# Performance work log

Measured on AMD Instinct MI355X. Metric: run time of the kernel, lower is better.

Reference implementation:

```python
import jax, jax.numpy as jnp
import numpy as np
from jax import lax

B, H, N, F = 32, 168, 512, 8
P_STEPS = 24


def setup_inputs() -> dict:
    key = jax.random.key(0)
    ks = jax.random.split(key, 8)
    s = 0.02
    return {
        "x": jax.random.normal(ks[0], (B, H, N, F), dtype=jnp.float32),
        "conv_w": jax.random.normal(ks[1], (N * F, N), dtype=jnp.float32) * s,
        "conv_b": jnp.zeros((N,), dtype=jnp.float32),
        "lstm_k": jax.random.normal(ks[2], (N, 4 * N), dtype=jnp.float32) * s,
        "lstm_rk": jax.random.normal(ks[3], (N, 4 * N), dtype=jnp.float32) * s,
        "lstm_b": jnp.zeros((4 * N,), dtype=jnp.float32),
        "dense_w": jax.random.normal(ks[4], (N, N), dtype=jnp.float32) * s,
        "dense_b": jnp.zeros((N,), dtype=jnp.float32),
        "P": P_STEPS,
    }


def _lstm_cell(h, c, x_t, lstm_k, lstm_rk, lstm_b):
    # Keras LSTMCell gate order: i, f, g(candidate), o
    z = x_t @ lstm_k + h @ lstm_rk + lstm_b  # [B, 4N]
    i, f, g, o = jnp.split(z, 4, axis=-1)
    i = jax.nn.sigmoid(i)
    f = jax.nn.sigmoid(f)
    g = jnp.tanh(g)
    o = jax.nn.sigmoid(o)
    c_new = f * c + i * g
    h_new = o * jnp.tanh(c_new)
    return h_new, c_new


def reference(x, conv_w, conv_b, lstm_k, lstm_rk, lstm_b, dense_w, dense_b, P):
    b, hh, n, f = x.shape
    # Conv1D kernel_size=1 == per-timestep dense projection N*F -> N
    xr = x.reshape(b, hh, n * f) @ conv_w + conv_b  # [B, H, N]

    h0 = jnp.zeros((b, n), dtype=x.dtype)
    c0 = jnp.zeros((b, n), dtype=x.dtype)

    def enc_step(carry, x_t):
        h, c = carry
        h, c = _lstm_cell(h, c, x_t, lstm_k, lstm_rk, lstm_b)
        return (h, c), None

    (h, c), _ = lax.scan(enc_step, (h0, c0), xr.transpose(1, 0, 2))

    def dec_step(carry, _):
        h, c = carry
        h2, c2 = _lstm_cell(h, c, h, lstm_k, lstm_rk, lstm_b)
        return (h2, c2), h2

    _, preds = lax.scan(dec_step, (h, c), None, length=P)  # [P, B, N]
    preds = preds.transpose(1, 0, 2)  # [B, P, N]
    return preds @ dense_w + dense_b
```

## Files before the change

### kernel.cpp

```cpp
#include <hip/hip_runtime.h>
#include <hip/hip_bf16.h>
#include <math.h>

typedef __hip_bfloat16 bf16;
typedef __attribute__((ext_vector_type(8))) short short8;
typedef __attribute__((ext_vector_type(4))) float floatx4;

#define B_  32
#define H_  168
#define N_  512
#define P_  24
#define NF_ 4096
#define G4N 2048
#define M1  (B_*H_)
#define NX  (M1*NF_)
#define TSTEPS (H_+P_)
#define NWG 64
#define HSZ (B_*N_)

__global__ __launch_bounds__(256) void cvt_f32_bf16(const float* __restrict__ in,
                                                    bf16* __restrict__ out, int n4) {
  int i = blockIdx.x * 256 + threadIdx.x;
  if (i < n4) {
    float4 v = ((const float4*)in)[i];
    bf16 o[4] = {__float2bfloat16(v.x), __float2bfloat16(v.y),
                 __float2bfloat16(v.z), __float2bfloat16(v.w)};
    *(ulong1*)(out + (size_t)i * 4) = *(ulong1*)o;
  }
}

__global__ __launch_bounds__(256) void transpose_cvt(const float* __restrict__ in,
                                                     bf16* __restrict__ out,
                                                     int R, int C) {
  __shared__ float t[32][33];
  int bx = blockIdx.x, by = blockIdx.y;
  int tx = threadIdx.x, ty = threadIdx.y;
#pragma unroll
  for (int yy = 0; yy < 32; yy += 8)
    t[ty + yy][tx] = in[(size_t)(by * 32 + ty + yy) * C + bx * 32 + tx];
  __syncthreads();
#pragma unroll
  for (int yy = 0; yy < 32; yy += 8)
    out[(size_t)(bx * 32 + ty + yy) * R + by * 32 + tx] =
        __float2bfloat16(t[tx][ty + yy]);
}

__global__ __launch_bounds__(256) void transpose_add_cvt(const float* __restrict__ in1,
                                                         const float* __restrict__ in2,
                                                         bf16* __restrict__ out,
                                                         int R, int C) {
  __shared__ float t[32][33];
  int bx = blockIdx.x, by = blockIdx.y;
  int tx = threadIdx.x, ty = threadIdx.y;
#pragma unroll
  for (int yy = 0; yy < 32; yy += 8) {
    size_t idx = (size_t)(by * 32 + ty + yy) * C + bx * 32 + tx;
    t[ty + yy][tx] = in1[idx] + in2[idx];
  }
  __syncthreads();
#pragma unroll
  for (int yy = 0; yy < 32; yy += 8)
    out[(size_t)(bx * 32 + ty + yy) * R + by * 32 + tx] =
        __float2bfloat16(t[tx][ty + yy]);
}

template <bool OUT_BF16>
__global__ __launch_bounds__(256) void gemm_bt(const bf16* __restrict__ A,
                                               const bf16* __restrict__ BT,
                                               const float* __restrict__ bias,
                                               void* __restrict__ Cout,
                                               int M, int N, int K, int permute) {
  __shared__ short As[128 * 40];
  __shared__ short Bs[128 * 40];
  int tid  = threadIdx.x;
  int wave = tid >> 6, lane = tid & 63;
  int wm = wave >> 1, wn = wave & 1;
  int quad = lane >> 4, l16 = lane & 15;
  int m0 = blockIdx.y * 128, n0 = blockIdx.x * 128;

  floatx4 acc[4][4];
#pragma unroll
  for (int i = 0; i < 4; i++)
#pragma unroll
    for (int j = 0; j < 4; j++) acc[i][j] = (floatx4){0.f, 0.f, 0.f, 0.f};

  int r0 = tid >> 2;
  int c0 = (tid & 3) * 8;

  for (int k0 = 0; k0 < K; k0 += 32) {
    short8 a0 = *(const short8*)(A  + (size_t)(m0 + r0)      * K + k0 + c0);
    short8 a1 = *(const short8*)(A  + (size_t)(m0 + r0 + 64) * K + k0 + c0);
    short8 b0 = *(const short8*)(BT + (size_t)(n0 + r0)      * K + k0 + c0);
    short8 b1 = *(const short8*)(BT + (size_t)(n0 + r0 + 64) * K + k0 + c0);
    __syncthreads();
    *(short8*)(&As[r0 * 40 + c0])        = a0;
    *(short8*)(&As[(r0 + 64) * 40 + c0]) = a1;
    *(short8*)(&Bs[r0 * 40 + c0])        = b0;
    *(short8*)(&Bs[(r0 + 64) * 40 + c0]) = b1;
    __syncthreads();
    short8 af[4], bfr[4];
#pragma unroll
    for (int i = 0; i < 4; i++)
      af[i] = *(const short8*)(&As[(wm * 64 + i * 16 + l16) * 40 + quad * 8]);
#pragma unroll
    for (int j = 0; j < 4; j++)
      bfr[j] = *(const short8*)(&Bs[(wn * 64 + j * 16 + l16) * 40 + quad * 8]);
#pragma unroll
    for (int i = 0; i < 4; i++)
#pragma unroll
      for (int j = 0; j < 4; j++)
        acc[i][j] = __builtin_amdgcn_mfma_f32_16x16x32_bf16(af[i], bfr[j],
                                                            acc[i][j], 0, 0, 0);
  }
#pragma unroll
  for (int i = 0; i < 4; i++) {
    int row = m0 + wm * 64 + i * 16 + quad * 4;
#pragma unroll
    for (int j = 0; j < 4; j++) {
      int col = n0 + wn * 64 + j * 16 + l16;
      float bv = bias ? bias[col] : 0.f;
#pragma unroll
      for (int r = 0; r < 4; r++) {
        int gr = row + r;
        int orow = permute ? (gr % H_) * B_ + gr / H_ : gr;
        float v = acc[i][j][r] + bv;
        if (OUT_BF16)
          ((bf16*)Cout)[(size_t)orow * N + col] = __float2bfloat16(v);
        else
          ((float*)Cout)[(size_t)orow * N + col] = v;
      }
    }
  }
}

__global__ __launch_bounds__(256) void lstm_persist(
    const bf16* __restrict__ rkT,
    const bf16* __restrict__ wcT,
    const float* __restrict__ bvec,
    const float* __restrict__ xk,
    bf16* __restrict__ hring,
    bf16* __restrict__ preds,
    unsigned* __restrict__ bar,
    unsigned* __restrict__ flag) {
  __shared__ short Wenc[32][520];
  __shared__ short Wdec[32][520];
  __shared__ float zs[32][33];
  __shared__ bf16  hstage[32][8];

  int tid  = threadIdx.x;
  int wave = tid >> 6, lane = tid & 63;
  int tm = wave >> 1, tn = wave & 1;
  int quad = lane >> 4, l16 = lane & 15;
  int n0 = blockIdx.x * 8;
  int lc   = tn * 16 + l16;
  int gcol = ((lc >> 3) << 9) + n0 + (lc & 7);
  int brow = tm * 16 + quad * 4;

  for (int idx = tid; idx < 32 * 64; idx += 256) {
    int r = idx >> 6, ck = (idx & 63) << 3;
    int grow = ((r >> 3) << 9) + n0 + (r & 7);
    *(short8*)&Wenc[r][ck] = *(const short8*)(rkT + (size_t)grow * 512 + ck);
    *(short8*)&Wdec[r][ck] = *(const short8*)(wcT + (size_t)grow * 512 + ck);
  }
  float bias_r = bvec[gcol];
  int b = tid >> 3, j = tid & 7;
  int nn = n0 + j;
  float c_reg = 0.f;

  float xkv[4];
  {
    const float* xp = xk + (size_t)brow * G4N + gcol;
#pragma unroll
    for (int r = 0; r < 4; ++r) xkv[r] = xp[(size_t)r * G4N];
  }
  __syncthreads();

  for (int t = 0; t < TSTEPS; ++t) {
    const bf16* h_in = hring + (size_t)t * HSZ;
    bf16*       h_out = hring + (size_t)(t + 1) * HSZ;
    const short(*Ws)[520] = (t < H_) ? Wenc : Wdec;

    floatx4 acc0 = (floatx4){0.f, 0.f, 0.f, 0.f};
    floatx4 acc1 = (floatx4){0.f, 0.f, 0.f, 0.f};
    const bf16*  ap = h_in + (size_t)(tm * 16 + l16) * 512 + quad * 8;
    const short* bp = &Ws[lc][quad * 8];
#pragma unroll
    for (int k0 = 0; k0 < 512; k0 += 64) {
      short8 av0 = *(const short8*)(ap + k0);
      short8 av1 = *(const short8*)(ap + k0 + 32);
      short8 bv0 = *(const short8*)(bp + k0);
      short8 bv1 = *(const short8*)(bp + k0 + 32);
      acc0 = __builtin_amdgcn_mfma_f32_16x16x32_bf16(av0, bv0, acc0, 0, 0, 0);
      acc1 = __builtin_amdgcn_mfma_f32_16x16x32_bf16(av1, bv1, acc1, 0, 0, 0);
    }
    floatx4 acc = acc0 + acc1;
#pragma unroll
    for (int r = 0; r < 4; ++r)
      zs[brow + r][lc] = acc[r] + bias_r + xkv[r];

    float xn[4] = {0.f, 0.f, 0.f, 0.f};
    if (t + 1 < H_) {
      const float* xp = xk + (size_t)((t + 1) * B_ + brow) * G4N + gcol;
#pragma unroll
      for (int r = 0; r < 4; ++r) xn[r] = xp[(size_t)r * G4N];
    }
    __syncthreads();

    float zi = zs[b][j], zf = zs[b][8 + j], zg = zs[b][16 + j], zo = zs[b][24 + j];
    float ig = 1.f / (1.f + __expf(-zi));
    float fg = 1.f / (1.f + __expf(-zf));
    float gg = tanhf(zg);
    float og = 1.f / (1.f + __expf(-zo));
    c_reg = fg * c_reg + ig * gg;
    float hn = og * tanhf(c_reg);
    hstage[b][j] = __float2bfloat16(hn);
    if (t >= H_)
      preds[(size_t)b * (P_ * N_) + (t - H_) * N_ + nn] = __float2bfloat16(hn);
    __syncthreads();

    if (tid < 64) {
      int bb = tid >> 1, f4 = (tid & 1) * 4;
      unsigned long long v = *(const unsigned long long*)&hstage[bb][f4];
      __hip_atomic_store((unsigned long long*)(h_out + bb * 512 + n0 + f4), v,
                         __ATOMIC_RELAXED, __HIP_MEMORY_SCOPE_AGENT);
    }
    __syncthreads();

    if (tid == 0) {
      unsigned old = __hip_atomic_fetch_add(&bar[t], 1u, __ATOMIC_RELAXED,
                                            __HIP_MEMORY_SCOPE_AGENT);
      if (old == NWG - 1) {
        __hip_atomic_store(&flag[t], 1u, __ATOMIC_RELAXED,
                           __HIP_MEMORY_SCOPE_AGENT);
      } else {
        while (!__hip_atomic_load(&flag[t], __ATOMIC_RELAXED,
                                  __HIP_MEMORY_SCOPE_AGENT))
          __builtin_amdgcn_s_sleep(1);
      }
    }
    __builtin_amdgcn_fence(__ATOMIC_ACQUIRE, "workgroup");
    __syncthreads();
#pragma unroll
    for (int r = 0; r < 4; ++r) xkv[r] = xn[r];
  }
}

extern "C" void kernel_launch(void* const* d_in, const int* in_sizes, int n_in,
                              void* d_out, int out_size, void* d_ws, size_t ws_size,
                              hipStream_t stream) {
  const float* x       = (const float*)d_in[0];
  const float* conv_w  = (const float*)d_in[1];
  const float* conv_b  = (const float*)d_in[2];
  const float* lstm_k  = (const float*)d_in[3];
  const float* lstm_rk = (const float*)d_in[4];
  const float* lstm_b  = (const float*)d_in[5];
  const float* dense_w = (const float*)d_in[6];
  const float* dense_b = (const float*)d_in[7];
  float* out = (float*)d_out;

  char* p = (char*)d_ws;
  auto carve = [&](size_t bytes) {
    char* r = p;
    p += (bytes + 255) & ~(size_t)255;
    return r;
  };
  bf16*  xb    = (bf16*)carve((size_t)NX * 2);
  bf16*  xr    = (bf16*)carve((size_t)M1 * N_ * 2);
  float* xk    = (float*)carve((size_t)M1 * G4N * 4);
  bf16*  cwT   = (bf16*)carve((size_t)N_ * NF_ * 2);
  bf16*  kT    = (bf16*)carve((size_t)G4N * N_ * 2);
  bf16*  rkT   = (bf16*)carve((size_t)G4N * N_ * 2);
  bf16*  wcT   = (bf16*)carve((size_t)G4N * N_ * 2);
  bf16*  dwT   = (bf16*)carve((size_t)N_ * N_ * 2);
  bf16*  preds = (bf16*)carve((size_t)B_ * P_ * N_ * 2);
  bf16*  hring = (bf16*)carve((size_t)(TSTEPS + 1) * HSZ * 2);
  unsigned* bar  = (unsigned*)carve((size_t)TSTEPS * 4);
  unsigned* flag = (unsigned*)carve((size_t)TSTEPS * 4);

  cvt_f32_bf16<<<(NX / 4 + 255) / 256, 256, 0, stream>>>(x, xb, NX / 4);
  dim3 tb(32, 8);
  transpose_cvt<<<dim3(N_ / 32, NF_ / 32), tb, 0, stream>>>(conv_w, cwT, NF_, N_);
  transpose_cvt<<<dim3(G4N / 32, N_ / 32), tb, 0, stream>>>(lstm_k, kT, N_, G4N);
  transpose_cvt<<<dim3(G4N / 32, N_ / 32), tb, 0, stream>>>(lstm_rk, rkT, N_, G4N);
  transpose_add_cvt<<<dim3(G4N / 32, N_ / 32), tb, 0, stream>>>(lstm_k, lstm_rk,
                                                                wcT, N_, G4N);
  transpose_cvt<<<dim3(N_ / 32, N_ / 32), tb, 0, stream>>>(dense_w, dwT, N_, N_);
  hipMemsetAsync(hring, 0, (size_t)HSZ * 2, stream);
  hipMemsetAsync(bar, 0, (size_t)TSTEPS * 4, stream);
  hipMemsetAsync(flag, 0, (size_t)TSTEPS * 4, stream);

  gemm_bt<true><<<dim3(N_ / 128, M1 / 128), 256, 0, stream>>>(xb, cwT, conv_b, xr,
                                                              M1, N_, NF_, 1);
  gemm_bt<false><<<dim3(G4N / 128, M1 / 128), 256, 0, stream>>>(xr, kT, nullptr,
                                                                xk, M1, G4N, N_, 0);

  lstm_persist<<<NWG, 256, 0, stream>>>(rkT, wcT, lstm_b, xk, hring, preds,
                                        bar, flag);

  gemm_bt<false><<<dim3(N_ / 128, (B_ * P_) / 128), 256, 0, stream>>>(
      preds, dwT, dense_b, out, B_ * P_, N_, N_, 0);
}
```

Before: 1.065 ms.

## Replace atomic-counter grid barrier with per-wave byte flags polled in parallel

Each wave now writes its h values directly with per-element atomic stores and then sets its own byte flag for the step. One wave of every workgroup polls all 256 flags as 64 packed words, one per lane. This replaces the LDS staging, two block syncs, the serialized fetch_add counter and the single release flag. The next-step xk prefetch is moved to after the flag write so its latency overlaps the barrier wait. In exchange the h writes are 2-byte scattered atomic stores instead of 8-byte ones, and correctness relies on s_waitcnt ordering the data stores before the flag store.

```diff
diff --git a/kernel.cpp b/kernel.cpp
--- a/kernel.cpp
+++ b/kernel.cpp
@@ -140,12 +140,10 @@
     const float* __restrict__ xk,
     bf16* __restrict__ hring,
     bf16* __restrict__ preds,
-    unsigned* __restrict__ bar,
-    unsigned* __restrict__ flag) {
+    unsigned char* __restrict__ flg) {
   __shared__ short Wenc[32][520];
   __shared__ short Wdec[32][520];
   __shared__ float zs[32][33];
-  __shared__ bf16  hstage[32][8];
 
   int tid  = threadIdx.x;
   int wave = tid >> 6, lane = tid & 63;
@@ -176,7 +174,7 @@
   __syncthreads();
 
   for (int t = 0; t < TSTEPS; ++t) {
-    const bf16* h_in = hring + (size_t)t * HSZ;
+    const bf16* h_in  = hring + (size_t)t * HSZ;
     bf16*       h_out = hring + (size_t)(t + 1) * HSZ;
     const short(*Ws)[520] = (t < H_) ? Wenc : Wdec;
 
@@ -197,13 +195,6 @@
 #pragma unroll
     for (int r = 0; r < 4; ++r)
       zs[brow + r][lc] = acc[r] + bias_r + xkv[r];
-
-    float xn[4] = {0.f, 0.f, 0.f, 0.f};
-    if (t + 1 < H_) {
-      const float* xp = xk + (size_t)((t + 1) * B_ + brow) * G4N + gcol;
-#pragma unroll
-      for (int r = 0; r < 4; ++r) xn[r] = xp[(size_t)r * G4N];
-    }
     __syncthreads();
 
     float zi = zs[b][j], zf = zs[b][8 + j], zg = zs[b][16 + j], zo = zs[b][24 + j];
@@ -213,30 +204,31 @@
     float og = 1.f / (1.f + __expf(-zo));
     c_reg = fg * c_reg + ig * gg;
     float hn = og * tanhf(c_reg);
-    hstage[b][j] = __float2bfloat16(hn);
+    bf16 hv = __float2bfloat16(hn);
+    unsigned short hu = *(unsigned short*)&hv;
+    __hip_atomic_store((unsigned short*)h_out + (size_t)b * 512 + nn, hu,
+                       __ATOMIC_RELAXED, __HIP_MEMORY_SCOPE_AGENT);
     if (t >= H_)
-      preds[(size_t)b * (P_ * N_) + (t - H_) * N_ + nn] = __float2bfloat16(hn);
-    __syncthreads();
-
-    if (tid < 64) {
-      int bb = tid >> 1, f4 = (tid & 1) * 4;
-      unsigned long long v = *(const unsigned long long*)&hstage[bb][f4];
-      __hip_atomic_store((unsigned long long*)(h_out + bb * 512 + n0 + f4), v,
-                         __ATOMIC_RELAXED, __HIP_MEMORY_SCOPE_AGENT);
-    }
-    __syncthreads();
-
-    if (tid == 0) {
-      unsigned old = __hip_atomic_fetch_add(&bar[t], 1u, __ATOMIC_RELAXED,
-                                            __HIP_MEMORY_SCOPE_AGENT);
-      if (old == NWG - 1) {
-        __hip_atomic_store(&flag[t], 1u, __ATOMIC_RELAXED,
-                           __HIP_MEMORY_SCOPE_AGENT);
-      } else {
-        while (!__hip_atomic_load(&flag[t], __ATOMIC_RELAXED,
-                                  __HIP_MEMORY_SCOPE_AGENT))
-          __builtin_amdgcn_s_sleep(1);
-      }
+      preds[(size_t)b * (P_ * N_) + (t - H_) * N_ + nn] = hv;
+
+    asm volatile("s_waitcnt vmcnt(0)" ::: "memory");
+    if (lane == 0)
+      __hip_atomic_store(flg + (size_t)t * 256 + blockIdx.x * 4 + wave,
+                         (unsigned char)1, __ATOMIC_RELAXED,
+                         __HIP_MEMORY_SCOPE_AGENT);
+
+    float xn[4] = {0.f, 0.f, 0.f, 0.f};
+    if (t + 1 < H_) {
+      const float* xp = xk + (size_t)((t + 1) * B_ + brow) * G4N + gcol;
+#pragma unroll
+      for (int r = 0; r < 4; ++r) xn[r] = xp[(size_t)r * G4N];
+    }
+
+    if (wave == 0) {
+      const unsigned* fp = (const unsigned*)(flg + (size_t)t * 256) + lane;
+      while (__hip_atomic_load(fp, __ATOMIC_RELAXED,
+                               __HIP_MEMORY_SCOPE_AGENT) != 0x01010101u)
+        __builtin_amdgcn_s_sleep(1);
     }
     __builtin_amdgcn_fence(__ATOMIC_ACQUIRE, "workgroup");
     __syncthreads();
@@ -274,8 +266,7 @@
   bf16*  dwT   = (bf16*)carve((size_t)N_ * N_ * 2);
   bf16*  preds = (bf16*)carve((size_t)B_ * P_ * N_ * 2);
   bf16*  hring = (bf16*)carve((size_t)(TSTEPS + 1) * HSZ * 2);
-  unsigned* bar  = (unsigned*)carve((size_t)TSTEPS * 4);
-  unsigned* flag = (unsigned*)carve((size_t)TSTEPS * 4);
+  unsigned char* flg = (unsigned char*)carve((size_t)TSTEPS * 256);
 
   cvt_f32_bf16<<<(NX / 4 + 255) / 256, 256, 0, stream>>>(x, xb, NX / 4);
   dim3 tb(32, 8);
@@ -286,16 +277,14 @@
                                                                 wcT, N_, G4N);
   transpose_cvt<<<dim3(N_ / 32, N_ / 32), tb, 0, stream>>>(dense_w, dwT, N_, N_);
   hipMemsetAsync(hring, 0, (size_t)HSZ * 2, stream);
-  hipMemsetAsync(bar, 0, (size_t)TSTEPS * 4, stream);
-  hipMemsetAsync(flag, 0, (size_t)TSTEPS * 4, stream);
+  hipMemsetAsync(flg, 0, (size_t)TSTEPS * 256, stream);
 
   gemm_bt<true><<<dim3(N_ / 128, M1 / 128), 256, 0, stream>>>(xb, cwT, conv_b, xr,
                                                               M1, N_, NF_, 1);
   gemm_bt<false><<<dim3(G4N / 128, M1 / 128), 256, 0, stream>>>(xr, kT, nullptr,
                                                                 xk, M1, G4N, N_, 0);
 
-  lstm_persist<<<NWG, 256, 0, stream>>>(rkT, wcT, lstm_b, xk, hring, preds,
-                                        bar, flag);
+  lstm_persist<<<NWG, 256, 0, stream>>>(rkT, wcT, lstm_b, xk, hring, preds, flg);
 
   gemm_bt<false><<<dim3(N_ / 128, (B_ * P_) / 128), 256, 0, stream>>>(
       preds, dwT, dense_b, out, B_ * P_, N_, N_, 0);
```

Measured after the change: 1.796 ms. 68.6% more time.
